# Performance work log

Measured on AMD Instinct MI355X. Metric: run time of the kernel, lower is better.

Reference implementation:

```python
import jax, jax.numpy as jnp
import numpy as np

N_EMBD = 1024
N_HEAD = 16


def setup_inputs() -> dict:
    key = jax.random.key(0)
    k1, k2, k3, k4, k5 = jax.random.split(key, 5)
    B, T, C = 4, 2048, N_EMBD
    s = 1.0 / np.sqrt(C)
    x = jax.random.normal(k1, (B, T, C), dtype=jnp.float32)
    w_weight = jax.random.normal(k2, (3 * C, C), dtype=jnp.float32) * s
    w_bias = jax.random.normal(k3, (3 * C,), dtype=jnp.float32) * s
    proj_weight = jax.random.normal(k4, (C, C), dtype=jnp.float32) * s
    proj_bias = jax.random.normal(k5, (C,), dtype=jnp.float32) * s
    return {"x": x, "w_weight": w_weight, "w_bias": w_bias,
            "proj_weight": proj_weight, "proj_bias": proj_bias}


def reference(x, w_weight, w_bias, proj_weight, proj_bias):
    B, T, C = x.shape
    nh = N_HEAD
    hs = C // nh
    # fused QKV projection (torch Linear: x @ W^T + b)
    wei = jnp.einsum('btc,oc->bto', x, w_weight) + w_bias
    k, q, v = jnp.split(wei, 3, axis=-1)  # note: chunk order is k, q, v
    # [B, T, nh, hs] -> [B, nh, T, hs]
    key_ = k.reshape(B, T, nh, hs).transpose(0, 2, 1, 3)
    query = q.reshape(B, T, nh, hs).transpose(0, 2, 1, 3)
    value = v.reshape(B, T, nh, hs).transpose(0, 2, 1, 3)
    scale = hs ** (-0.5)
    weight = jnp.einsum('bhqd,bhkd->bhqk', query, key_) * scale
    weight = jax.nn.softmax(weight, axis=-1)
    out = jnp.einsum('bhqk,bhkd->bhqd', weight, value)  # [B, nh, T, hs]
    # Faithful to source bug: transpose(1,2) is discarded; view is taken on
    # the (B, nh, T, hs) layout directly.
    out = out.reshape(B, T, C)
    out = jnp.einsum('btc,oc->bto', out, proj_weight) + proj_bias
    return out
```

## Files before the change

kernel.cpp:

```cpp
#include <hip/hip_runtime.h>
#include <hip/hip_bf16.h>


typedef __attribute__((ext_vector_type(8)))  short bf16x8;
typedef __attribute__((ext_vector_type(4)))  float f32x4;
typedef __attribute__((ext_vector_type(16))) float f32x16;
typedef __attribute__((ext_vector_type(2)))  unsigned u32x2;

typedef __attribute__((address_space(3))) unsigned lds_u32_t;
typedef __attribute__((address_space(1))) unsigned glb_u32_t;

__device__ __forceinline__ void async_cp16(const short* g, short* l) {
    __builtin_amdgcn_global_load_lds((glb_u32_t*)g, (lds_u32_t*)l, 16, 0, 0);
}

__device__ __forceinline__ float exp2fast(float x) {
    return __builtin_amdgcn_exp2f(x);
}

__device__ __forceinline__ short f2bf(float f) {
    union { float f; unsigned u; } v; v.f = f;
    unsigned r = v.u + 0x7fffu + ((v.u >> 16) & 1u);
    return (short)(r >> 16);
}

__device__ __forceinline__ unsigned cvt_pk_bf16(float lo, float hi) {
    unsigned r;
    asm("v_cvt_pk_bf16_f32 %0, %1, %2" : "=v"(r) : "v"(lo), "v"(hi));
    return r;
}

__global__ __launch_bounds__(256) void cvt_kernel(const float4* __restrict__ in,
                                                  short4* __restrict__ out, int n4) {
    int i = blockIdx.x * 256 + threadIdx.x;
    if (i < n4) {
        float4 v = in[i];
        short4 o;
        o.x = f2bf(v.x); o.y = f2bf(v.y); o.z = f2bf(v.z); o.w = f2bf(v.w);
        out[i] = o;
    }
}

template<int EPI>
__global__ __launch_bounds__(256) void gemm_bf16(
    const short* __restrict__ A, const short* __restrict__ W,
    const float* __restrict__ bias, float* __restrict__ outF,
    short* __restrict__ kout, short* __restrict__ qout, short* __restrict__ vtout,
    int M, int N, int K)
{
    __shared__ short lA[2][128 * 64];
    __shared__ short lB[2][128 * 64];
    const int tid  = threadIdx.x;
    const int lane = tid & 63;
    const int wave = tid >> 6;
    const int wM = (wave >> 1) * 64;
    const int wN = (wave & 1) * 64;
    const int l15 = lane & 15, l4 = lane >> 4;
    const int rsw = (lane & 7) << 3;
    const int rowBase = blockIdx.y * 128;
    const int colBase = blockIdx.x * 128;

    auto STAGE = [&](int t, int buf) {
        const int k0 = t * 64;
        #pragma unroll
        for (int i = 0; i < 4; ++i) {
            int idx = i * 256 + tid;
            int r   = idx >> 3;
            int cp  = ((idx & 7) ^ (r & 7)) * 8;
            int eo  = idx * 8;
            async_cp16(A + (size_t)(rowBase + r) * K + k0 + cp, &lA[buf][eo]);
            async_cp16(W + (size_t)(colBase + r) * K + k0 + cp, &lB[buf][eo]);
        }
    };

    f32x4 acc[4][4] = {};
    const int NT = K >> 6;

    STAGE(0, 0);
    __syncthreads();

    int cur = 0;
    for (int t = 0; t < NT; ++t) {
        if (t + 1 < NT) STAGE(t + 1, cur ^ 1);
        #pragma unroll
        for (int kt = 0; kt < 2; ++kt) {
            bf16x8 af[4], bfr[4];
            #pragma unroll
            for (int mt = 0; mt < 4; ++mt)
                af[mt] = *(const bf16x8*)(
                    &lA[cur][(wM + mt * 16 + l15) * 64 + ((kt * 32 + l4 * 8) ^ rsw)]);
            #pragma unroll
            for (int nt = 0; nt < 4; ++nt)
                bfr[nt] = *(const bf16x8*)(
                    &lB[cur][(wN + nt * 16 + l15) * 64 + ((kt * 32 + l4 * 8) ^ rsw)]);
            #pragma unroll
            for (int mt = 0; mt < 4; ++mt)
                #pragma unroll
                for (int nt = 0; nt < 4; ++nt)
                    acc[mt][nt] = __builtin_amdgcn_mfma_f32_16x16x32_bf16(
                        af[mt], bfr[nt], acc[mt][nt], 0, 0, 0);
        }
        __syncthreads();
        cur ^= 1;
    }

    #pragma unroll
    for (int mt = 0; mt < 4; ++mt) {
        #pragma unroll
        for (int nt = 0; nt < 4; ++nt) {
            const int n  = colBase + wN + nt * 16 + l15;
            const int mb = rowBase + wM + mt * 16 + l4 * 4;
            const float bv = bias[n];
            #pragma unroll
            for (int r = 0; r < 4; ++r) {
                const int m = mb + r;
                float val = acc[mt][nt][r] + bv;
                if (EPI == 0) {
                    int b = m >> 11, t = m & 2047;
                    int j = n >> 10, hd = n & 1023;
                    int h = hd >> 6, d = hd & 63;
                    size_t base = ((size_t)(b * 16 + h) * 2048 + t) * 64 + d;
                    if (j == 0)      kout[base] = f2bf(val);
                    else if (j == 1) qout[base] = f2bf(val * 0.180336879f);
                    else             vtout[((size_t)(b * 16 + h) * 64 + d) * 2048 + t] = f2bf(val);
                } else {
                    outF[(size_t)m * N + n] = val;
                }
            }
        }
    }
}

__global__ __launch_bounds__(256) void attn_kernel(
    const short* __restrict__ Q, const short* __restrict__ Km,
    const short* __restrict__ Vt, short* __restrict__ O)
{
    __shared__ short kbuf[2][64 * 64];
    __shared__ short vbuf[2][64 * 64];

    const int tid  = threadIdx.x;
    const int lane = tid & 63;
    const int wave = tid >> 6;
    const int l31 = lane & 31;
    const int l1  = lane >> 5;

    const int b     = blockIdx.x;
    const int xcd   = b & 7;
    const int inner = b >> 3;
    const int bx    = inner & 15;
    const int bh    = xcd * 8 + (inner >> 4);
    const int q0    = bx * 128 + wave * 32;

    const short* Qh = Q  + (size_t)bh * 2048 * 64;
    const short* Kh = Km + (size_t)bh * 2048 * 64;
    const short* Vh = Vt + (size_t)bh * 64 * 2048;

    const int i8 = lane >> 3, i7 = lane & 7;
    const int srcCol = 8 * (i7 ^ i8);
    const int rsw    = (l31 & 7) << 3;

    auto STAGE = [&](int kv, int buf) {
        if (wave < 2) {
            #pragma unroll
            for (int c = 0; c < 4; ++c) {
                int j = wave * 4 + c;
                async_cp16(Kh + (size_t)(kv + 8 * j + i8) * 64 + srcCol,
                           &kbuf[buf][j * 512 + lane * 8]);
            }
        } else {
            #pragma unroll
            for (int c = 0; c < 4; ++c) {
                int j = (wave - 2) * 4 + c;
                async_cp16(Vh + (size_t)(8 * j + i8) * 2048 + kv + srcCol,
                           &vbuf[buf][j * 512 + lane * 8]);
            }
        }
    };

    bf16x8 qf[4];
    #pragma unroll
    for (int s = 0; s < 4; ++s)
        qf[s] = *(const bf16x8*)(Qh + (size_t)(q0 + l31) * 64 + s * 16 + l1 * 8);

    f32x16 o[2] = {};
    float l_run = 0.f;

    STAGE(0, 0);
    __syncthreads();

    int cur = 0;
    for (int it = 0; it < 32; ++it) {
        if (it < 31) STAGE((it + 1) * 64, cur ^ 1);

        f32x16 s2[2] = {};
        #pragma unroll
        for (int t = 0; t < 2; ++t) {
            #pragma unroll
            for (int s = 0; s < 4; ++s) {
                bf16x8 kf = *(const bf16x8*)(
                    &kbuf[cur][(t * 32 + l31) * 64 + ((s * 16 + l1 * 8) ^ rsw)]);
                s2[t] = __builtin_amdgcn_mfma_f32_32x32x16_bf16(kf, qf[s], s2[t], 0, 0, 0);
            }
        }

        float ps0 = 0.f, ps1 = 0.f, ps2 = 0.f, ps3 = 0.f;
        #pragma unroll
        for (int t = 0; t < 2; ++t)
            #pragma unroll
            for (int i = 0; i < 16; ++i) {
                float p = exp2fast(s2[t][i]);
                s2[t][i] = p;
                if ((i & 3) == 0) ps0 += p;
                else if ((i & 3) == 1) ps1 += p;
                else if ((i & 3) == 2) ps2 += p;
                else ps3 += p;
            }
        float ps = (ps0 + ps1) + (ps2 + ps3);
        ps += __shfl_xor(ps, 32);
        l_run += ps;

        bf16x8 pa[4];
        #pragma unroll
        for (int t = 0; t < 2; ++t) {
            #pragma unroll
            for (int sl = 0; sl < 2; ++sl) {
                unsigned A0 = cvt_pk_bf16(s2[t][8 * sl + 0], s2[t][8 * sl + 1]);
                unsigned A1 = cvt_pk_bf16(s2[t][8 * sl + 2], s2[t][8 * sl + 3]);
                unsigned B0 = cvt_pk_bf16(s2[t][8 * sl + 4], s2[t][8 * sl + 5]);
                unsigned B1 = cvt_pk_bf16(s2[t][8 * sl + 6], s2[t][8 * sl + 7]);
                u32x2 ra = __builtin_amdgcn_permlane32_swap(A0, B0, false, false);
                u32x2 rb = __builtin_amdgcn_permlane32_swap(A1, B1, false, false);
                union { unsigned u[4]; bf16x8 v; } w;
                w.u[0] = ra.x;
                w.u[1] = rb.x;
                w.u[2] = ra.y;
                w.u[3] = rb.y;
                pa[2 * t + sl] = w.v;
            }
        }

        #pragma unroll
        for (int s = 0; s < 4; ++s)
            #pragma unroll
            for (int dt = 0; dt < 2; ++dt) {
                bf16x8 vf = *(const bf16x8*)(
                    &vbuf[cur][(dt * 32 + l31) * 64 + ((s * 16 + l1 * 8) ^ rsw)]);
                o[dt] = __builtin_amdgcn_mfma_f32_32x32x16_bf16(pa[s], vf, o[dt], 0, 0, 0);
            }

        __syncthreads();
        cur ^= 1;
    }

    float invl = 1.f / l_run;
    #pragma unroll
    for (int g = 0; g < 4; ++g)
        #pragma unroll
        for (int rr = 0; rr < 4; ++rr) {
            float c = __shfl(invl, rr + 8 * g + 4 * l1);
            int qrow = q0 + rr + 8 * g + 4 * l1;
            size_t base = ((size_t)bh * 2048 + qrow) * 64 + l31;
            O[base]      = f2bf(o[0][g * 4 + rr] * c);
            O[base + 32] = f2bf(o[1][g * 4 + rr] * c);
        }
}

extern "C" void kernel_launch(void* const* d_in, const int* in_sizes, int n_in,
                              void* d_out, int out_size, void* d_ws, size_t ws_size,
                              hipStream_t stream) {
    const float* x  = (const float*)d_in[0];
    const float* ww = (const float*)d_in[1];
    const float* wb = (const float*)d_in[2];
    const float* pwt = (const float*)d_in[3];
    const float* pb  = (const float*)d_in[4];
    float* out = (float*)d_out;

    short* ws  = (short*)d_ws;
    short* xb  = ws;
    short* wwb = xb  + 8192 * 1024;
    short* pwb = wwb + 3072 * 1024;
    short* qb  = pwb + 1024 * 1024;
    short* kb  = qb  + 64 * 2048 * 64;
    short* vtb = kb  + 64 * 2048 * 64;
    short* ob  = vtb + 64 * 2048 * 64;

    cvt_kernel<<<2097152 / 256, 256, 0, stream>>>((const float4*)x,  (short4*)xb,  2097152);
    cvt_kernel<<< 786432 / 256, 256, 0, stream>>>((const float4*)ww, (short4*)wwb,  786432);
    cvt_kernel<<< 262144 / 256, 256, 0, stream>>>((const float4*)pwt,(short4*)pwb,  262144);

    gemm_bf16<0><<<dim3(24, 64), 256, 0, stream>>>(
        xb, wwb, wb, nullptr, kb, qb, vtb, 8192, 3072, 1024);

    attn_kernel<<<1024, 256, 0, stream>>>(qb, kb, vtb, ob);

    gemm_bf16<1><<<dim3(8, 64), 256, 0, stream>>>(
        ob, pwb, pb, out, nullptr, nullptr, nullptr, 8192, 1024, 1024);
}
```

Before: 222.1 us.

## Compute softmax row sums via MFMA with ones vector, add setprio and incremental staging pointers

The attention kernel drops the per-element VALU accumulation of exp values and the cross-lane shuffle. Instead it computes the row sums with an extra MFMA against a vector of bf16 ones, accumulating in a matrix register that already has the output layout. It also wraps the MFMA blocks in s_setprio raises and precomputes the async-copy source and destination pointers, advancing them by a fixed stride each tile. This trades VALU and shuffle work for more MFMA issue, and the denominator now sums bf16-rounded probabilities instead of fp32 ones.

Result: no change. 219.0 us (-1.4%).

```diff
diff --git a/kernel.cpp b/kernel.cpp
--- a/kernel.cpp
+++ b/kernel.cpp
@@ -159,21 +159,31 @@
     const int srcCol = 8 * (i7 ^ i8);
     const int rsw    = (l31 & 7) << 3;
 
-    auto STAGE = [&](int kv, int buf) {
-        if (wave < 2) {
-            #pragma unroll
-            for (int c = 0; c < 4; ++c) {
-                int j = wave * 4 + c;
-                async_cp16(Kh + (size_t)(kv + 8 * j + i8) * 64 + srcCol,
-                           &kbuf[buf][j * 512 + lane * 8]);
-            }
-        } else {
-            #pragma unroll
-            for (int c = 0; c < 4; ++c) {
-                int j = (wave - 2) * 4 + c;
-                async_cp16(Vh + (size_t)(8 * j + i8) * 2048 + kv + srcCol,
-                           &vbuf[buf][j * 512 + lane * 8]);
-            }
+    const short* src[4];
+    short* dst0[4];
+    int step;
+    if (wave < 2) {
+        #pragma unroll
+        for (int c = 0; c < 4; ++c) {
+            int j = wave * 4 + c;
+            src[c]  = Kh + (size_t)(8 * j + i8) * 64 + srcCol;
+            dst0[c] = &kbuf[0][j * 512 + lane * 8];
+        }
+        step = 64 * 64;
+    } else {
+        #pragma unroll
+        for (int c = 0; c < 4; ++c) {
+            int j = (wave - 2) * 4 + c;
+            src[c]  = Vh + (size_t)(8 * j + i8) * 2048 + srcCol;
+            dst0[c] = &vbuf[0][j * 512 + lane * 8];
+        }
+        step = 64;
+    }
+    auto STAGE = [&](int buf) {
+        #pragma unroll
+        for (int c = 0; c < 4; ++c) {
+            async_cp16(src[c], dst0[c] + buf * 4096);
+            src[c] += step;
         }
     };
 
@@ -182,17 +192,23 @@
     for (int s = 0; s < 4; ++s)
         qf[s] = *(const bf16x8*)(Qh + (size_t)(q0 + l31) * 64 + s * 16 + l1 * 8);
 
+    union { unsigned u[4]; bf16x8 v; } onesu;
+    #pragma unroll
+    for (int j = 0; j < 4; ++j) onesu.u[j] = 0x3F803F80u;
+    const bf16x8 onesf = onesu.v;
+
     f32x16 o[2] = {};
-    float l_run = 0.f;
-
-    STAGE(0, 0);
+    f32x16 ol   = {};
+
+    STAGE(0);
     __syncthreads();
 
     int cur = 0;
     for (int it = 0; it < 32; ++it) {
-        if (it < 31) STAGE((it + 1) * 64, cur ^ 1);
+        if (it < 31) STAGE(cur ^ 1);
 
         f32x16 s2[2] = {};
+        __builtin_amdgcn_s_setprio(1);
         #pragma unroll
         for (int t = 0; t < 2; ++t) {
             #pragma unroll
@@ -202,22 +218,13 @@
                 s2[t] = __builtin_amdgcn_mfma_f32_32x32x16_bf16(kf, qf[s], s2[t], 0, 0, 0);
             }
         }
-
-        float ps0 = 0.f, ps1 = 0.f, ps2 = 0.f, ps3 = 0.f;
+        __builtin_amdgcn_s_setprio(0);
+
         #pragma unroll
         for (int t = 0; t < 2; ++t)
             #pragma unroll
-            for (int i = 0; i < 16; ++i) {
-                float p = exp2fast(s2[t][i]);
-                s2[t][i] = p;
-                if ((i & 3) == 0) ps0 += p;
-                else if ((i & 3) == 1) ps1 += p;
-                else if ((i & 3) == 2) ps2 += p;
-                else ps3 += p;
-            }
-        float ps = (ps0 + ps1) + (ps2 + ps3);
-        ps += __shfl_xor(ps, 32);
-        l_run += ps;
+            for (int i = 0; i < 16; ++i)
+                s2[t][i] = exp2fast(s2[t][i]);
 
         bf16x8 pa[4];
         #pragma unroll
@@ -239,29 +246,32 @@
             }
         }
 
-        #pragma unroll
-        for (int s = 0; s < 4; ++s)
+        __builtin_amdgcn_s_setprio(1);
+        #pragma unroll
+        for (int s = 0; s < 4; ++s) {
             #pragma unroll
             for (int dt = 0; dt < 2; ++dt) {
                 bf16x8 vf = *(const bf16x8*)(
                     &vbuf[cur][(dt * 32 + l31) * 64 + ((s * 16 + l1 * 8) ^ rsw)]);
                 o[dt] = __builtin_amdgcn_mfma_f32_32x32x16_bf16(pa[s], vf, o[dt], 0, 0, 0);
             }
+            ol = __builtin_amdgcn_mfma_f32_32x32x16_bf16(pa[s], onesf, ol, 0, 0, 0);
+        }
+        __builtin_amdgcn_s_setprio(0);
 
         __syncthreads();
         cur ^= 1;
     }
 
-    float invl = 1.f / l_run;
     #pragma unroll
     for (int g = 0; g < 4; ++g)
         #pragma unroll
         for (int rr = 0; rr < 4; ++rr) {
-            float c = __shfl(invl, rr + 8 * g + 4 * l1);
+            float invl = 1.f / ol[g * 4 + rr];
             int qrow = q0 + rr + 8 * g + 4 * l1;
             size_t base = ((size_t)bh * 2048 + qrow) * 64 + l31;
-            O[base]      = f2bf(o[0][g * 4 + rr] * c);
-            O[base + 32] = f2bf(o[1][g * 4 + rr] * c);
+            O[base]      = f2bf(o[0][g * 4 + rr] * invl);
+            O[base + 32] = f2bf(o[1][g * 4 + rr] * invl);
         }
 }
 
```
